# Kernel optimization log

Hardware: AMD Instinct MI355X
Metric: run time of the kernel (lower is better)

## Reference

```python
import jax, jax.numpy as jnp
import numpy as np

B, S, HID = 2, 4096, 2048
NH, NKV, HD = 32, 8, 64
GROUPS = NH // NKV
ROPE_THETA = 10000.0


def _rope_cos_sin(seq_len, dim, dtype):
    inv_freq = 1.0 / (ROPE_THETA ** (jnp.arange(0, dim, 2, dtype=jnp.float32) / dim))
    pos = jnp.arange(seq_len, dtype=jnp.float32)
    freqs = pos[:, None] * inv_freq[None, :]          # [S, D/2]
    emb = jnp.concatenate([freqs, freqs], axis=-1)    # [S, D]
    return jnp.cos(emb).astype(dtype), jnp.sin(emb).astype(dtype)


def _rotate_half(x):
    x1, x2 = jnp.split(x, 2, axis=-1)
    return jnp.concatenate([-x2, x1], axis=-1)


def _apply_rope(x, cos, sin):
    # x: [B, H, S, D]; cos/sin: [S, D]
    return x * cos[None, None] + _rotate_half(x) * sin[None, None]


def kappa(x):
    return jax.nn.elu(x) + 1.0


def setup_inputs() -> dict:
    key = jax.random.key(0)
    ks = jax.random.split(key, 6)
    sc = 0.02
    return {
        "hidden_states": jax.random.normal(ks[0], (B, S, HID), jnp.float32),
        "Wq": jax.random.normal(ks[1], (HID, NH * HD), jnp.float32) * sc,
        "Wk": jax.random.normal(ks[2], (HID, NKV * HD), jnp.float32) * sc,
        "Wv": jax.random.normal(ks[3], (HID, NKV * HD), jnp.float32) * sc,
        "Wphi": jax.random.normal(ks[4], (HID, HID), jnp.float32) * sc,
        "Wo": jax.random.normal(ks[5], (HID, HID), jnp.float32) * sc,
    }


def reference(hidden_states, Wq, Wk, Wv, Wphi, Wo):
    bsz, q_len, _ = hidden_states.shape

    q = (hidden_states @ Wq).reshape(bsz, q_len, NH, HD).transpose(0, 2, 1, 3)   # [B,NH,S,D]
    k = (hidden_states @ Wk).reshape(bsz, q_len, NKV, HD).transpose(0, 2, 1, 3)  # [B,NKV,S,D]
    v = (hidden_states @ Wv).reshape(bsz, q_len, NKV, HD).transpose(0, 2, 1, 3)

    cos, sin = _rope_cos_sin(q_len, HD, hidden_states.dtype)
    q = _apply_rope(q, cos, sin)
    k = _apply_rope(k, cos, sin)

    # repeat_kv for GQA: [B,NKV,S,D] -> [B,NH,S,D]
    k = jnp.repeat(k, GROUPS, axis=1)
    v = jnp.repeat(v, GROUPS, axis=1)

    Qk = kappa(q)   # [B,NH,S,D]
    Kk = kappa(k)

    Qg = Qk.mean(axis=2)                                # [B,NH,D] global query
    logits = jnp.einsum("bnd,bnsd->bns", Qg, Kk)        # [B,NH,S]
    alpha = jax.nn.softmax(logits, axis=-1) * float(q_len)

    # KV aggregation: [B,NH,D,D] state
    outer_sum = jnp.einsum("bns,bnsd,bnsf->bndf", alpha, Kk, v)
    result_attn = jnp.einsum("bnsd,bndf->bnsf", Qk, outer_sum)  # [B,NH,S,D]

    X_phi = (hidden_states @ Wphi).reshape(bsz, q_len, NH, HD).transpose(0, 2, 1, 3)
    ctx = (X_phi * result_attn).transpose(0, 2, 1, 3).reshape(bsz, q_len, HID)
    return ctx @ Wo
```

## Files before the change

### kernel.cpp

```cpp
#include <hip/hip_runtime.h>
#include <hip/hip_bf16.h>

#define B_ 2
#define S_ 4096
#define HID_ 2048
#define NH_ 32
#define NKV_ 8
#define HD_ 64
#define GROUPS_ 4
#define NCH_ 32

typedef short short8 __attribute__((ext_vector_type(8)));
typedef float floatx4 __attribute__((ext_vector_type(4)));

__device__ __forceinline__ float bf2f(unsigned short u){
  union { unsigned int i; float f; } v; v.i = ((unsigned int)u) << 16; return v.f;
}
__device__ __forceinline__ unsigned short f2bf(float f){
  union { float f; unsigned int i; } v; v.f = f;
  unsigned int i = v.i;
  unsigned int r = (i + 0x7fffu + ((i >> 16) & 1u)) >> 16;
  return (unsigned short)r;
}

__device__ __forceinline__ void async_copy16(unsigned short* lds, const unsigned short* g){
  __builtin_amdgcn_global_load_lds((const __attribute__((address_space(1))) void*)g,
                                   (__attribute__((address_space(3))) void*)lds,
                                   16, 0, 0);
}

__global__ void conv_bf16(const float* __restrict__ x, unsigned short* __restrict__ y, int n4){
  int i = blockIdx.x * 256 + threadIdx.x;
  if (i < n4){
    float4 v = ((const float4*)x)[i];
    ushort4 o;
    o.x = f2bf(v.x); o.y = f2bf(v.y); o.z = f2bf(v.z); o.w = f2bf(v.w);
    ((ushort4*)y)[i] = o;
  }
}

__global__ void transpose_to_bf16(const float* __restrict__ W, unsigned short* __restrict__ Wt,
                                  int K, int N){
  __shared__ float tile[32][33];
  int n0 = blockIdx.x * 32, k0 = blockIdx.y * 32;
  int tx = threadIdx.x, ty = threadIdx.y;
  #pragma unroll
  for (int j = 0; j < 4; j++)
    tile[ty + j*8][tx] = W[(size_t)(k0 + ty + j*8) * N + n0 + tx];
  __syncthreads();
  #pragma unroll
  for (int j = 0; j < 4; j++)
    Wt[(size_t)(n0 + ty + j*8) * K + k0 + tx] = f2bf(tile[tx][ty + j*8]);
}

#define GTILE 16384

__global__ __launch_bounds__(512, 2) void gemm256(
    const unsigned short* __restrict__ A, const unsigned short* __restrict__ Bt,
    float* __restrict__ C, int M, int N, int K)
{
  __shared__ __align__(16) unsigned short As[2 * GTILE];
  __shared__ __align__(16) unsigned short Bs[2 * GTILE];

  const int tid = threadIdx.x;
  const int w = tid >> 6, lane = tid & 63;
  const int wr = w >> 2, wc = w & 3;
  const int l15 = lane & 15, quad = lane >> 4;

  const int nbx = N >> 8;
  int flat = blockIdx.y * nbx + blockIdx.x;
  int nwg  = nbx * (M >> 8);
  int cpx  = nwg >> 3;
  int swz  = (flat & 7) * cpx + (flat >> 3);
  int bx = swz % nbx, by = swz / nbx;
  const int m0 = by << 8, n0 = bx << 8;

  const int srow = (w << 3) + (lane >> 3);
  const int scc  = (lane & 7) ^ (lane >> 3);
  const unsigned short* gA = A  + (size_t)(m0 + srow) * K + scc * 8;
  const unsigned short* gB = Bt + (size_t)(n0 + srow) * K + scc * 8;
  const size_t rs64  = (size_t)64  * K;
  const size_t rs128 = (size_t)128 * K;
  unsigned short* lA0 = As + (w << 9);
  unsigned short* lB0 = Bs + (w << 9);

#define STAGE_A(bsel, h, t) do { \
    unsigned short* _d = lA0 + (bsel) * GTILE + (h) * 8192; \
    const unsigned short* _g = gA + (size_t)(h) * rs128 + (size_t)(t) * 64; \
    async_copy16(_d, _g); \
    async_copy16(_d + 4096, _g + rs64); \
  } while (0)
#define STAGE_B(bsel, h, t) do { \
    unsigned short* _d = lB0 + (bsel) * GTILE + (h) * 8192; \
    const unsigned short* _g = gB + (size_t)(h) * rs128 + (size_t)(t) * 64; \
    async_copy16(_d, _g); \
    async_copy16(_d + 4096, _g + rs64); \
  } while (0)
#define SCHED0 __builtin_amdgcn_sched_barrier(0)

  const int ks0  = ((quad     ^ (lane & 7)) << 3);
  const int ks1  = (((4+quad) ^ (lane & 7)) << 3);
  const int arow = (wr * 128 + l15) * 64;
  const int brow = (wc * 64  + l15) * 64;

  floatx4 acc[8][4] = {};
  short8 af[8][2], bfr[4][2];

  const int nt = K >> 6;

  STAGE_A(0, 0, 0); STAGE_A(0, 1, 0); STAGE_B(0, 0, 0); STAGE_B(0, 1, 0);
  if (nt > 1){
    STAGE_A(1, 0, 1); STAGE_A(1, 1, 1); STAGE_B(1, 0, 1); STAGE_B(1, 1, 1);
    asm volatile("s_waitcnt vmcnt(8)" ::: "memory");
  } else {
    asm volatile("s_waitcnt vmcnt(0)" ::: "memory");
  }
  SCHED0;
  __builtin_amdgcn_s_barrier();
  SCHED0;

  for (int T = 0; T < nt; ++T){
    const int cb = T & 1;
    const unsigned short* Ab = As + cb * GTILE;
    const unsigned short* Bb = Bs + cb * GTILE;

    #pragma unroll
    for (int m = 0; m < 4; ++m){
      af[m][0] = *(const short8*)(Ab + arow + m * 1024 + ks0);
      af[m][1] = *(const short8*)(Ab + arow + m * 1024 + ks1);
    }
    #pragma unroll
    for (int n = 0; n < 2; ++n){
      bfr[n][0] = *(const short8*)(Bb + brow + n * 1024 + ks0);
      bfr[n][1] = *(const short8*)(Bb + brow + n * 1024 + ks1);
    }
    SCHED0; __builtin_amdgcn_s_barrier(); SCHED0;
    __builtin_amdgcn_s_setprio(1);
    #pragma unroll
    for (int m = 0; m < 4; ++m)
      #pragma unroll
      for (int n = 0; n < 2; ++n){
        acc[m][n] = __builtin_amdgcn_mfma_f32_16x16x32_bf16(af[m][0], bfr[n][0], acc[m][n], 0, 0, 0);
        acc[m][n] = __builtin_amdgcn_mfma_f32_16x16x32_bf16(af[m][1], bfr[n][1], acc[m][n], 0, 0, 0);
      }
    __builtin_amdgcn_s_setprio(0);
    SCHED0; __builtin_amdgcn_s_barrier(); SCHED0;

    #pragma unroll
    for (int m = 0; m < 4; ++m){
      af[4+m][0] = *(const short8*)(Ab + arow + (4+m) * 1024 + ks0);
      af[4+m][1] = *(const short8*)(Ab + arow + (4+m) * 1024 + ks1);
    }
    #pragma unroll
    for (int n = 0; n < 2; ++n){
      bfr[2+n][0] = *(const short8*)(Bb + brow + (2+n) * 1024 + ks0);
      bfr[2+n][1] = *(const short8*)(Bb + brow + (2+n) * 1024 + ks1);
    }
    SCHED0; __builtin_amdgcn_s_barrier(); SCHED0;
    __builtin_amdgcn_s_setprio(1);
    #pragma unroll
    for (int m = 0; m < 4; ++m)
      #pragma unroll
      for (int n = 0; n < 2; ++n){
        acc[m][2+n] = __builtin_amdgcn_mfma_f32_16x16x32_bf16(af[m][0], bfr[2+n][0], acc[m][2+n], 0, 0, 0);
        acc[m][2+n] = __builtin_amdgcn_mfma_f32_16x16x32_bf16(af[m][1], bfr[2+n][1], acc[m][2+n], 0, 0, 0);
      }
    __builtin_amdgcn_s_setprio(0);
    SCHED0; __builtin_amdgcn_s_barrier(); SCHED0;

    if (T + 2 < nt){ STAGE_A(cb, 0, T + 2); STAGE_A(cb, 1, T + 2); }
    SCHED0; __builtin_amdgcn_s_barrier(); SCHED0;
    __builtin_amdgcn_s_setprio(1);
    #pragma unroll
    for (int m = 0; m < 4; ++m)
      #pragma unroll
      for (int n = 0; n < 2; ++n){
        acc[4+m][n] = __builtin_amdgcn_mfma_f32_16x16x32_bf16(af[4+m][0], bfr[n][0], acc[4+m][n], 0, 0, 0);
        acc[4+m][n] = __builtin_amdgcn_mfma_f32_16x16x32_bf16(af[4+m][1], bfr[n][1], acc[4+m][n], 0, 0, 0);
      }
    __builtin_amdgcn_s_setprio(0);
    SCHED0; __builtin_amdgcn_s_barrier(); SCHED0;

    if (T + 2 < nt){
      STAGE_B(cb, 0, T + 2); STAGE_B(cb, 1, T + 2);
      asm volatile("s_waitcnt vmcnt(8)" ::: "memory");
    } else {
      asm volatile("s_waitcnt vmcnt(0)" ::: "memory");
    }
    SCHED0; __builtin_amdgcn_s_barrier(); SCHED0;
    __builtin_amdgcn_s_setprio(1);
    #pragma unroll
    for (int m = 0; m < 4; ++m)
      #pragma unroll
      for (int n = 0; n < 2; ++n){
        acc[4+m][2+n] = __builtin_amdgcn_mfma_f32_16x16x32_bf16(af[4+m][0], bfr[2+n][0], acc[4+m][2+n], 0, 0, 0);
        acc[4+m][2+n] = __builtin_amdgcn_mfma_f32_16x16x32_bf16(af[4+m][1], bfr[2+n][1], acc[4+m][2+n], 0, 0, 0);
      }
    __builtin_amdgcn_s_setprio(0);
    SCHED0; __builtin_amdgcn_s_barrier(); SCHED0;
  }

#undef STAGE_A
#undef STAGE_B
#undef SCHED0

  #pragma unroll
  for (int mi = 0; mi < 8; ++mi){
    const int row = m0 + wr * 128 + mi * 16 + quad * 4;
    #pragma unroll
    for (int ni = 0; ni < 4; ++ni){
      const int col = n0 + wc * 64 + ni * 16 + l15;
      #pragma unroll
      for (int r = 0; r < 4; ++r)
        C[(size_t)(row + r) * N + col] = acc[mi][ni][r];
    }
  }
}

__global__ void rope_kappa_q(const float* __restrict__ Qlin, unsigned short* __restrict__ Qk){
  int idx = blockIdx.x * 256 + threadIdx.x;
  int i = idx & 31;
  int n = (idx >> 5) & (NH_ - 1);
  int s = (idx >> 10) & (S_ - 1);
  int b = idx >> 22;
  float invf = exp2f(-(float)i * (13.287712379549449f / 32.0f));
  float ang = (float)s * invf;
  float c = cosf(ang), sn = sinf(ang);
  size_t in_o = ((size_t)(b * S_ + s) * NH_ + n) * HD_;
  float x1 = Qlin[in_o + i];
  float x2 = Qlin[in_o + i + 32];
  float r1 = x1 * c - x2 * sn;
  float r2 = x2 * c + x1 * sn;
  r1 = r1 > 0.f ? r1 + 1.f : __expf(r1);
  r2 = r2 > 0.f ? r2 + 1.f : __expf(r2);
  size_t o = ((size_t)(b * NH_ + n) * S_ + s) * HD_;
  Qk[o + i] = f2bf(r1);
  Qk[o + i + 32] = f2bf(r2);
}

__global__ void rope_kappa_k(const float* __restrict__ KVlin, unsigned short* __restrict__ Kk){
  int idx = blockIdx.x * 256 + threadIdx.x;
  int i = idx & 31;
  int kv = (idx >> 5) & (NKV_ - 1);
  int s = (idx >> 8) & (S_ - 1);
  int b = idx >> 20;
  float invf = exp2f(-(float)i * (13.287712379549449f / 32.0f));
  float ang = (float)s * invf;
  float c = cosf(ang), sn = sinf(ang);
  size_t in_o = (size_t)(b * S_ + s) * 1024 + kv * HD_;
  float x1 = KVlin[in_o + i];
  float x2 = KVlin[in_o + i + 32];
  float r1 = x1 * c - x2 * sn;
  float r2 = x2 * c + x1 * sn;
  r1 = r1 > 0.f ? r1 + 1.f : __expf(r1);
  r2 = r2 > 0.f ? r2 + 1.f : __expf(r2);
  size_t o = ((size_t)(b * NKV_ + kv) * S_ + s) * HD_;
  Kk[o + i] = f2bf(r1);
  Kk[o + i + 32] = f2bf(r2);
}

__global__ __launch_bounds__(256) void qg_mean(const unsigned short* __restrict__ Qk,
                                               float* __restrict__ Qg){
  int bn = blockIdx.x, chunk = blockIdx.y;
  int tid = threadIdx.x;
  int dgrp = tid & 7, sgrp = tid >> 3;
  const unsigned short* base = Qk + (size_t)bn * S_ * HD_
                             + (size_t)(chunk * 256 + sgrp) * HD_ + dgrp * 8;
  float acc[8] = {};
  #pragma unroll
  for (int i = 0; i < 8; i++){
    short8 v = *(const short8*)(base + (size_t)i * 32 * HD_);
    #pragma unroll
    for (int e = 0; e < 8; e++) acc[e] += bf2f((unsigned short)v[e]);
  }
  __shared__ float red[256][8];
  #pragma unroll
  for (int e = 0; e < 8; e++) red[tid][e] = acc[e];
  __syncthreads();
  if (tid < 64){
    int dg = tid >> 3, e = tid & 7;
    float s = 0.f;
    #pragma unroll
    for (int g = 0; g < 32; g++) s += red[g * 8 + dg][e];
    atomicAdd(&Qg[bn * 64 + tid], s * (1.0f / (float)S_));
  }
}

__global__ __launch_bounds__(256) void logits_kernel(const unsigned short* __restrict__ Kk,
                                                     const float* __restrict__ Qg,
                                                     float* __restrict__ logits){
  int bn = blockIdx.x, chunk = blockIdx.y;
  int b = bn / NH_, n = bn % NH_, kv = n / GROUPS_;
  int tid = threadIdx.x;
  __shared__ float qg[64];
  if (tid < 64) qg[tid] = Qg[bn * 64 + tid];
  __syncthreads();
  int s = chunk * 256 + tid;
  const unsigned short* row = Kk + ((size_t)(b * NKV_ + kv) * S_ + s) * HD_;
  float acc = 0.f;
  #pragma unroll
  for (int c = 0; c < 8; c++){
    short8 v = *(const short8*)(row + c * 8);
    #pragma unroll
    for (int e = 0; e < 8; e++) acc += qg[c * 8 + e] * bf2f((unsigned short)v[e]);
  }
  logits[(size_t)bn * S_ + s] = acc;
}

__global__ __launch_bounds__(256) void softmax_kernel(const float* __restrict__ logits,
                                                      float* __restrict__ alpha){
  int bn = blockIdx.x;
  int tid = threadIdx.x;
  float l[16];
  float mymax = -1e30f;
  #pragma unroll
  for (int j = 0; j < 16; j++){
    l[j] = logits[(size_t)bn * S_ + j * 256 + tid];
    mymax = fmaxf(mymax, l[j]);
  }
  __shared__ float red[256];
  red[tid] = mymax; __syncthreads();
  for (int st = 128; st > 0; st >>= 1){
    if (tid < st) red[tid] = fmaxf(red[tid], red[tid + st]);
    __syncthreads();
  }
  float gmax = red[0];
  __syncthreads();
  float mysum = 0.f;
  #pragma unroll
  for (int j = 0; j < 16; j++){ l[j] = __expf(l[j] - gmax); mysum += l[j]; }
  red[tid] = mysum; __syncthreads();
  for (int st = 128; st > 0; st >>= 1){
    if (tid < st) red[tid] += red[tid + st];
    __syncthreads();
  }
  float inv = (float)S_ / red[0];
  #pragma unroll
  for (int j = 0; j < 16; j++)
    alpha[(size_t)bn * S_ + j * 256 + tid] = l[j] * inv;
}

__global__ __launch_bounds__(256) void outer_sum_kernel(const unsigned short* __restrict__ Kk,
                                                        const float* __restrict__ KVlin,
                                                        const float* __restrict__ alpha,
                                                        float* __restrict__ part){
  int bkv = blockIdx.x, chunk = blockIdx.y;
  int b = bkv >> 3, kv = bkv & 7;
  int tid = threadIdx.x;
  int d = tid >> 2, fb = (tid & 3) * 16;
  __shared__ float ks[64][64];
  __shared__ float vs[64][64];
  __shared__ float as[4][64];
  float acc[4][16] = {};
  const unsigned short* kb = Kk + (size_t)(b * NKV_ + kv) * S_ * HD_;
  const int SPC = S_ / NCH_;

  for (int t = 0; t < SPC / 64; t++){
    int ss = chunk * SPC + t * 64;
    #pragma unroll
    for (int j = 0; j < 16; j++){
      int idx = j * 256 + tid;
      int si = idx >> 6, dd = idx & 63;
      ks[si][dd] = bf2f(kb[(size_t)(ss + si) * HD_ + dd]);
      vs[si][dd] = KVlin[(size_t)(b * S_ + ss + si) * 1024 + 512 + kv * HD_ + dd];
    }
    {
      int h = tid >> 6, si = tid & 63;
      as[h][si] = alpha[(size_t)(b * NH_ + kv * GROUPS_ + h) * S_ + ss + si];
    }
    __syncthreads();
    #pragma unroll 4
    for (int si = 0; si < 64; si++){
      float k = ks[si][d];
      float4 v0 = *(const float4*)&vs[si][fb];
      float4 v1 = *(const float4*)&vs[si][fb + 4];
      float4 v2 = *(const float4*)&vs[si][fb + 8];
      float4 v3 = *(const float4*)&vs[si][fb + 12];
      #pragma unroll
      for (int h = 0; h < 4; h++){
        float ak = as[h][si] * k;
        acc[h][0]  += ak * v0.x; acc[h][1]  += ak * v0.y; acc[h][2]  += ak * v0.z; acc[h][3]  += ak * v0.w;
        acc[h][4]  += ak * v1.x; acc[h][5]  += ak * v1.y; acc[h][6]  += ak * v1.z; acc[h][7]  += ak * v1.w;
        acc[h][8]  += ak * v2.x; acc[h][9]  += ak * v2.y; acc[h][10] += ak * v2.z; acc[h][11] += ak * v2.w;
        acc[h][12] += ak * v3.x; acc[h][13] += ak * v3.y; acc[h][14] += ak * v3.z; acc[h][15] += ak * v3.w;
      }
    }
    __syncthreads();
  }

  #pragma unroll
  for (int h = 0; h < 4; h++){
    float* pb = part + ((size_t)(chunk * 16 + bkv) * 4 + h) * 4096 + d * 64 + fb;
    #pragma unroll
    for (int j = 0; j < 4; j++)
      *(float4*)&pb[j * 4] = *(float4*)&acc[h][j * 4];
  }
}

__global__ __launch_bounds__(256) void osum_reduce_t(const float* __restrict__ part,
                                                     unsigned short* __restrict__ osumb){
  int bn = blockIdx.x;
  int tid = threadIdx.x;
  __shared__ float os[64][65];
  const float4* p4 = (const float4*)part;
  #pragma unroll
  for (int r = 0; r < 4; r++){
    int idx4 = r * 256 + tid;
    float4 s = {0.f, 0.f, 0.f, 0.f};
    #pragma unroll 8
    for (int c = 0; c < NCH_; c++){
      float4 v = p4[(size_t)c * 65536 + bn * 1024 + idx4];
      s.x += v.x; s.y += v.y; s.z += v.z; s.w += v.w;
    }
    int d = idx4 >> 4;
    int f0 = (idx4 & 15) * 4;
    os[d][f0] = s.x; os[d][f0+1] = s.y; os[d][f0+2] = s.z; os[d][f0+3] = s.w;
  }
  __syncthreads();
  int f = tid >> 2, d0 = (tid & 3) * 16;
  unsigned short hi[16], lo[16];
  #pragma unroll
  for (int j = 0; j < 16; j++){
    float x = os[d0 + j][f];
    unsigned short h = f2bf(x);
    hi[j] = h;
    lo[j] = f2bf(x - bf2f(h));
  }
  unsigned short* oh = osumb + ((size_t)bn * 2) * 4096 + (size_t)f * 64 + d0;
  unsigned short* ol = oh + 4096;
  *(short8*)(oh)     = *(const short8*)(hi);
  *(short8*)(oh + 8) = *(const short8*)(hi + 8);
  *(short8*)(ol)     = *(const short8*)(lo);
  *(short8*)(ol + 8) = *(const short8*)(lo + 8);
}

__global__ __launch_bounds__(256) void ctx_mfma(const unsigned short* __restrict__ Qk,
                                                const unsigned short* __restrict__ osumb,
                                                const float* __restrict__ Xphi,
                                                unsigned short* __restrict__ ctx){
  int bn = blockIdx.x, sc = blockIdx.y;
  int b = bn >> 5, n = bn & 31;
  int tid = threadIdx.x;
  int w = tid >> 6, lane = tid & 63;
  int l15 = lane & 15, quad = lane >> 4;

  const unsigned short* obase = osumb + ((size_t)bn * 2) * 4096;
  short8 bh[4][2], bl[4][2];
  #pragma unroll
  for (int nf = 0; nf < 4; nf++){
    int f = nf * 16 + l15;
    #pragma unroll
    for (int kh = 0; kh < 2; kh++){
      bh[nf][kh] = *(const short8*)(obase + (size_t)f * 64 + kh * 32 + quad * 8);
      bl[nf][kh] = *(const short8*)(obase + 4096 + (size_t)f * 64 + kh * 32 + quad * 8);
    }
  }

  int s0 = sc * 256 + w * 64;
  const unsigned short* qbase = Qk + ((size_t)bn * S_ + s0) * HD_;
  floatx4 acc[4][4] = {};
  #pragma unroll
  for (int m = 0; m < 4; m++){
    short8 a0 = *(const short8*)(qbase + (size_t)(m * 16 + l15) * HD_ + quad * 8);
    short8 a1 = *(const short8*)(qbase + (size_t)(m * 16 + l15) * HD_ + 32 + quad * 8);
    #pragma unroll
    for (int nf = 0; nf < 4; nf++){
      acc[m][nf] = __builtin_amdgcn_mfma_f32_16x16x32_bf16(a0, bh[nf][0], acc[m][nf], 0, 0, 0);
      acc[m][nf] = __builtin_amdgcn_mfma_f32_16x16x32_bf16(a1, bh[nf][1], acc[m][nf], 0, 0, 0);
      acc[m][nf] = __builtin_amdgcn_mfma_f32_16x16x32_bf16(a0, bl[nf][0], acc[m][nf], 0, 0, 0);
      acc[m][nf] = __builtin_amdgcn_mfma_f32_16x16x32_bf16(a1, bl[nf][1], acc[m][nf], 0, 0, 0);
    }
  }

  #pragma unroll
  for (int m = 0; m < 4; m++){
    #pragma unroll
    for (int r = 0; r < 4; r++){
      int s = s0 + m * 16 + quad * 4 + r;
      const float* xp = Xphi + ((size_t)(b * S_ + s) * NH_ + n) * HD_;
      unsigned short* cp = ctx + (size_t)(b * S_ + s) * HID_ + n * HD_;
      #pragma unroll
      for (int nf = 0; nf < 4; nf++){
        int f = nf * 16 + l15;
        cp[f] = f2bf(xp[f] * acc[m][nf][r]);
      }
    }
  }
}

extern "C" void kernel_launch(void* const* d_in, const int* in_sizes, int n_in,
                              void* d_out, int out_size, void* d_ws, size_t ws_size,
                              hipStream_t stream) {
  const float* hs   = (const float*)d_in[0];
  const float* Wq   = (const float*)d_in[1];
  const float* Wk   = (const float*)d_in[2];
  const float* Wv   = (const float*)d_in[3];
  const float* Wphi = (const float*)d_in[4];
  const float* Wo   = (const float*)d_in[5];
  float* out = (float*)d_out;

  char* ws = (char*)d_ws;
  const size_t M = (size_t)B_ * S_;
  size_t off = 0;
  auto alloc = [&](size_t bytes){ size_t o = off; off += (bytes + 255) & ~(size_t)255; return o; };

  size_t off_hsb   = alloc(M * HID_ * 2);
  size_t off_wqt   = alloc((size_t)HID_ * HID_ * 2);
  size_t off_wkvt  = alloc((size_t)HID_ * 1024 * 2);
  size_t off_wpt   = alloc((size_t)HID_ * HID_ * 2);
  size_t off_wot   = alloc((size_t)HID_ * HID_ * 2);
  size_t off_qlin  = alloc(M * HID_ * 4);
  size_t off_kvlin = alloc(M * 1024 * 4);
  size_t off_qk    = alloc(M * HID_ * 2);
  size_t off_kk    = alloc(M * 512 * 2);
  size_t off_qg    = alloc(64 * 64 * 4);
  size_t off_alph  = alloc((size_t)B_ * NH_ * S_ * 4);
  size_t off_osumb = alloc((size_t)64 * 2 * 4096 * 2);
  size_t off_ctx   = off_kvlin;
  size_t off_part  = off_qlin;
  (void)ws_size;

  unsigned short* hsb  = (unsigned short*)(ws + off_hsb);
  unsigned short* wqt  = (unsigned short*)(ws + off_wqt);
  unsigned short* wkvt = (unsigned short*)(ws + off_wkvt);
  unsigned short* wpt  = (unsigned short*)(ws + off_wpt);
  unsigned short* wot  = (unsigned short*)(ws + off_wot);
  float* qlin  = (float*)(ws + off_qlin);
  float* kvlin = (float*)(ws + off_kvlin);
  unsigned short* qk = (unsigned short*)(ws + off_qk);
  unsigned short* kk = (unsigned short*)(ws + off_kk);
  float* qg   = (float*)(ws + off_qg);
  float* alph = (float*)(ws + off_alph);
  unsigned short* osumb = (unsigned short*)(ws + off_osumb);
  float* part = (float*)(ws + off_part);
  unsigned short* ctx = (unsigned short*)(ws + off_ctx);

  conv_bf16<<<(int)(M * HID_ / 4 / 256), 256, 0, stream>>>(hs, hsb, (int)(M * HID_ / 4));
  transpose_to_bf16<<<dim3(HID_/32, HID_/32), dim3(32,8), 0, stream>>>(Wq, wqt, HID_, HID_);
  transpose_to_bf16<<<dim3(512/32,  HID_/32), dim3(32,8), 0, stream>>>(Wk, wkvt, HID_, 512);
  transpose_to_bf16<<<dim3(512/32,  HID_/32), dim3(32,8), 0, stream>>>(Wv, wkvt + (size_t)512 * HID_, HID_, 512);
  transpose_to_bf16<<<dim3(HID_/32, HID_/32), dim3(32,8), 0, stream>>>(Wphi, wpt, HID_, HID_);
  transpose_to_bf16<<<dim3(HID_/32, HID_/32), dim3(32,8), 0, stream>>>(Wo, wot, HID_, HID_);
  gemm256<<<dim3(HID_/256, M/256), 512, 0, stream>>>(hsb, wqt, qlin, (int)M, HID_, HID_);
  gemm256<<<dim3(1024/256, M/256), 512, 0, stream>>>(hsb, wkvt, kvlin, (int)M, 1024, HID_);
  rope_kappa_q<<<(int)(M * NH_ * 32 / 256), 256, 0, stream>>>(qlin, qk);
  rope_kappa_k<<<(int)(M * NKV_ * 32 / 256), 256, 0, stream>>>(kvlin, kk);
  hipMemsetAsync(qg, 0, 64 * 64 * 4, stream);
  qg_mean<<<dim3(B_ * NH_, S_ / 256), 256, 0, stream>>>(qk, qg);
  logits_kernel<<<dim3(B_ * NH_, S_ / 256), 256, 0, stream>>>(kk, qg, alph);
  softmax_kernel<<<B_ * NH_, 256, 0, stream>>>(alph, alph);
  outer_sum_kernel<<<dim3(B_ * NKV_, NCH_), 256, 0, stream>>>(kk, kvlin, alph, part);
  osum_reduce_t<<<64, 256, 0, stream>>>(part, osumb);
  gemm256<<<dim3(HID_/256, M/256), 512, 0, stream>>>(hsb, wpt, qlin, (int)M, HID_, HID_);
  ctx_mfma<<<dim3(B_ * NH_, S_ / 64 / 4), 256, 0, stream>>>(qk, osumb, qlin, ctx);
  gemm256<<<dim3(HID_/256, M/256), 512, 0, stream>>>(ctx, wot, out, (int)M, HID_, HID_);
}
```

Before: 567.0 us.

## Software-pipeline LDS fragment loads across GEMM k-iterations

Restructures the bf16 MFMA GEMM main loop so the next tile's first A/B fragments are read from LDS during the final MFMA block of the current iteration. Fragment loads are split into smaller chunks spread between MFMA phases, and the order of global stage issues and the vmcnt waits is reworked. The goal is to hide LDS read latency behind matrix-core work and cut idle time at barriers. In exchange, the synchronisation on the double buffer becomes more delicate and register pressure may rise.

```diff
diff --git a/kernel.cpp b/kernel.cpp
--- a/kernel.cpp
+++ b/kernel.cpp
@@ -97,6 +97,7 @@
     async_copy16(_d + 4096, _g + rs64); \
   } while (0)
 #define SCHED0 __builtin_amdgcn_sched_barrier(0)
+#define BARRIER do { SCHED0; __builtin_amdgcn_s_barrier(); SCHED0; } while (0)
 
   const int ks0  = ((quad     ^ (lane & 7)) << 3);
   const int ks1  = (((4+quad) ^ (lane & 7)) << 3);
@@ -115,26 +116,37 @@
   } else {
     asm volatile("s_waitcnt vmcnt(0)" ::: "memory");
   }
+  BARRIER;
+  #pragma unroll
+  for (int m = 0; m < 4; ++m){
+    af[m][0] = *(const short8*)(As + arow + m * 1024 + ks0);
+    af[m][1] = *(const short8*)(As + arow + m * 1024 + ks1);
+  }
+  #pragma unroll
+  for (int n = 0; n < 2; ++n){
+    bfr[n][0] = *(const short8*)(Bs + brow + n * 1024 + ks0);
+    bfr[n][1] = *(const short8*)(Bs + brow + n * 1024 + ks1);
+  }
   SCHED0;
-  __builtin_amdgcn_s_barrier();
-  SCHED0;
 
   for (int T = 0; T < nt; ++T){
-    const int cb = T & 1;
-    const unsigned short* Ab = As + cb * GTILE;
-    const unsigned short* Bb = Bs + cb * GTILE;
-
-    #pragma unroll
-    for (int m = 0; m < 4; ++m){
+    const int p = T & 1;
+    const unsigned short* Ab = As + p * GTILE;
+    const unsigned short* Bb = Bs + p * GTILE;
+    const unsigned short* Aq = As + (p ^ 1) * GTILE;
+    const unsigned short* Bq = Bs + (p ^ 1) * GTILE;
+
+    #pragma unroll
+    for (int n = 2; n < 4; ++n){
+      bfr[n][0] = *(const short8*)(Bb + brow + n * 1024 + ks0);
+      bfr[n][1] = *(const short8*)(Bb + brow + n * 1024 + ks1);
+    }
+    #pragma unroll
+    for (int m = 4; m < 6; ++m){
       af[m][0] = *(const short8*)(Ab + arow + m * 1024 + ks0);
       af[m][1] = *(const short8*)(Ab + arow + m * 1024 + ks1);
     }
-    #pragma unroll
-    for (int n = 0; n < 2; ++n){
-      bfr[n][0] = *(const short8*)(Bb + brow + n * 1024 + ks0);
-      bfr[n][1] = *(const short8*)(Bb + brow + n * 1024 + ks1);
-    }
-    SCHED0; __builtin_amdgcn_s_barrier(); SCHED0;
+    BARRIER;
     __builtin_amdgcn_s_setprio(1);
     #pragma unroll
     for (int m = 0; m < 4; ++m)
@@ -144,65 +156,73 @@
         acc[m][n] = __builtin_amdgcn_mfma_f32_16x16x32_bf16(af[m][1], bfr[n][1], acc[m][n], 0, 0, 0);
       }
     __builtin_amdgcn_s_setprio(0);
-    SCHED0; __builtin_amdgcn_s_barrier(); SCHED0;
-
-    #pragma unroll
-    for (int m = 0; m < 4; ++m){
-      af[4+m][0] = *(const short8*)(Ab + arow + (4+m) * 1024 + ks0);
-      af[4+m][1] = *(const short8*)(Ab + arow + (4+m) * 1024 + ks1);
-    }
-    #pragma unroll
-    for (int n = 0; n < 2; ++n){
-      bfr[2+n][0] = *(const short8*)(Bb + brow + (2+n) * 1024 + ks0);
-      bfr[2+n][1] = *(const short8*)(Bb + brow + (2+n) * 1024 + ks1);
-    }
-    SCHED0; __builtin_amdgcn_s_barrier(); SCHED0;
+    BARRIER;
+
+    #pragma unroll
+    for (int m = 6; m < 8; ++m){
+      af[m][0] = *(const short8*)(Ab + arow + m * 1024 + ks0);
+      af[m][1] = *(const short8*)(Ab + arow + m * 1024 + ks1);
+    }
+    BARRIER;
     __builtin_amdgcn_s_setprio(1);
     #pragma unroll
     for (int m = 0; m < 4; ++m)
       #pragma unroll
-      for (int n = 0; n < 2; ++n){
-        acc[m][2+n] = __builtin_amdgcn_mfma_f32_16x16x32_bf16(af[m][0], bfr[2+n][0], acc[m][2+n], 0, 0, 0);
-        acc[m][2+n] = __builtin_amdgcn_mfma_f32_16x16x32_bf16(af[m][1], bfr[2+n][1], acc[m][2+n], 0, 0, 0);
+      for (int n = 2; n < 4; ++n){
+        acc[m][n] = __builtin_amdgcn_mfma_f32_16x16x32_bf16(af[m][0], bfr[n][0], acc[m][n], 0, 0, 0);
+        acc[m][n] = __builtin_amdgcn_mfma_f32_16x16x32_bf16(af[m][1], bfr[n][1], acc[m][n], 0, 0, 0);
       }
     __builtin_amdgcn_s_setprio(0);
-    SCHED0; __builtin_amdgcn_s_barrier(); SCHED0;
-
-    if (T + 2 < nt){ STAGE_A(cb, 0, T + 2); STAGE_A(cb, 1, T + 2); }
-    SCHED0; __builtin_amdgcn_s_barrier(); SCHED0;
-    __builtin_amdgcn_s_setprio(1);
-    #pragma unroll
-    for (int m = 0; m < 4; ++m)
-      #pragma unroll
-      for (int n = 0; n < 2; ++n){
-        acc[4+m][n] = __builtin_amdgcn_mfma_f32_16x16x32_bf16(af[4+m][0], bfr[n][0], acc[4+m][n], 0, 0, 0);
-        acc[4+m][n] = __builtin_amdgcn_mfma_f32_16x16x32_bf16(af[4+m][1], bfr[n][1], acc[4+m][n], 0, 0, 0);
-      }
-    __builtin_amdgcn_s_setprio(0);
-    SCHED0; __builtin_amdgcn_s_barrier(); SCHED0;
+    BARRIER;
 
     if (T + 2 < nt){
-      STAGE_B(cb, 0, T + 2); STAGE_B(cb, 1, T + 2);
-      asm volatile("s_waitcnt vmcnt(8)" ::: "memory");
+      STAGE_A(p, 0, T + 2); STAGE_A(p, 1, T + 2);
+      asm volatile("s_waitcnt vmcnt(4)" ::: "memory");
     } else {
       asm volatile("s_waitcnt vmcnt(0)" ::: "memory");
     }
-    SCHED0; __builtin_amdgcn_s_barrier(); SCHED0;
+    BARRIER;
     __builtin_amdgcn_s_setprio(1);
     #pragma unroll
-    for (int m = 0; m < 4; ++m)
+    for (int m = 4; m < 8; ++m)
       #pragma unroll
       for (int n = 0; n < 2; ++n){
-        acc[4+m][2+n] = __builtin_amdgcn_mfma_f32_16x16x32_bf16(af[4+m][0], bfr[2+n][0], acc[4+m][2+n], 0, 0, 0);
-        acc[4+m][2+n] = __builtin_amdgcn_mfma_f32_16x16x32_bf16(af[4+m][1], bfr[2+n][1], acc[4+m][2+n], 0, 0, 0);
+        acc[m][n] = __builtin_amdgcn_mfma_f32_16x16x32_bf16(af[m][0], bfr[n][0], acc[m][n], 0, 0, 0);
+        acc[m][n] = __builtin_amdgcn_mfma_f32_16x16x32_bf16(af[m][1], bfr[n][1], acc[m][n], 0, 0, 0);
       }
     __builtin_amdgcn_s_setprio(0);
-    SCHED0; __builtin_amdgcn_s_barrier(); SCHED0;
+    BARRIER;
+
+    if (T + 2 < nt){ STAGE_B(p, 0, T + 2); STAGE_B(p, 1, T + 2); }
+    if (T + 1 < nt){
+      #pragma unroll
+      for (int m = 0; m < 4; ++m){
+        af[m][0] = *(const short8*)(Aq + arow + m * 1024 + ks0);
+        af[m][1] = *(const short8*)(Aq + arow + m * 1024 + ks1);
+      }
+      #pragma unroll
+      for (int n = 0; n < 2; ++n){
+        bfr[n][0] = *(const short8*)(Bq + brow + n * 1024 + ks0);
+        bfr[n][1] = *(const short8*)(Bq + brow + n * 1024 + ks1);
+      }
+    }
+    BARRIER;
+    __builtin_amdgcn_s_setprio(1);
+    #pragma unroll
+    for (int m = 4; m < 8; ++m)
+      #pragma unroll
+      for (int n = 2; n < 4; ++n){
+        acc[m][n] = __builtin_amdgcn_mfma_f32_16x16x32_bf16(af[m][0], bfr[n][0], acc[m][n], 0, 0, 0);
+        acc[m][n] = __builtin_amdgcn_mfma_f32_16x16x32_bf16(af[m][1], bfr[n][1], acc[m][n], 0, 0, 0);
+      }
+    __builtin_amdgcn_s_setprio(0);
+    BARRIER;
   }
 
 #undef STAGE_A
 #undef STAGE_B
 #undef SCHED0
+#undef BARRIER
 
   #pragma unroll
   for (int mi = 0; mi < 8; ++mi){
```

New measurement: 737.9 us. 30.1% more time.
